# Performance work log

Measured on AMD Instinct MI355X. Metric: run time of the kernel, lower is better.

Reference implementation:

```python
import jax, jax.numpy as jnp
import numpy as np

HID, NH, HD, MD = 512, 8, 64, 16  # hidden_dim, num_heads, head_dim, manifold_dim
B, S = 4, 1024
FLOW_STEPS, DT = 10, 0.1
EPS = 1e-8


def _cplx_weight(k, shape, std=0.02):
    kr, ki = jax.random.split(k)
    w = jax.random.normal(kr, shape) + 1j * jax.random.normal(ki, shape)
    return (w * std).astype(jnp.complex64)


def setup_inputs() -> dict:
    key = jax.random.key(0)
    ks = jax.random.split(key, 12)
    inp = {}
    inp['x_real'] = jax.random.normal(ks[0], (B, S, HID), dtype=jnp.float32)
    inp['x_imag'] = jax.random.normal(ks[1], (B, S, HID), dtype=jnp.float32)
    # manifold projection head_dim -> manifold_dim
    inp['Wm'] = _cplx_weight(ks[2], (MD, HD), std=HD ** -0.5)
    inp['bm'] = jnp.zeros((MD,), jnp.complex64)
    inp['Wq'] = _cplx_weight(ks[3], (MD, MD))
    inp['bq'] = jnp.zeros((MD,), jnp.complex64)
    inp['Wk'] = _cplx_weight(ks[4], (MD, MD))
    inp['bk'] = jnp.zeros((MD,), jnp.complex64)
    inp['Wv'] = _cplx_weight(ks[5], (MD, MD))
    inp['bv'] = jnp.zeros((MD,), jnp.complex64)
    # learned manifold metric (initialized to identity as in the module)
    inp['metric'] = jnp.eye(MD, dtype=jnp.complex64)
    # output projection expanded_dim = NH*MD -> hidden_dim
    inp['Wo'] = _cplx_weight(ks[6], (HID, NH * MD))
    inp['bo'] = jnp.zeros((HID,), jnp.complex64)
    return inp


def _forward(x_real, x_imag, Wm, bm, Wq, bq, Wk, bk, Wv, bv, metric, Wo, bo):
    x = (x_real + 1j * x_imag).astype(jnp.complex64)            # [B,S,HID]
    b, s, _ = x.shape
    h = x.reshape(b, s, NH, HD).transpose(0, 2, 1, 3)           # [B,NH,S,HD]
    # project onto low-dim manifold coordinates
    m = h @ Wm.T + bm                                           # [B,NH,S,MD]
    # hyperbolic exponential map at origin (curvature -1): tanh(|v|)/|v| * v
    n = jnp.sqrt(jnp.sum(jnp.abs(m) ** 2, -1, keepdims=True)) + EPS
    m = (jnp.tanh(n) / n) * m
    # parallel transport via the learned metric
    m = m @ metric
    # geometric flow: 10 Euler integration steps with dt=0.1
    sym = 0.5 * (metric + metric.conj().T)

    def step(carry, _):
        vel = carry @ sym - carry
        return carry + DT * vel, None

    m, _ = jax.lax.scan(step, m, None, length=FLOW_STEPS)
    # hyperbolic logarithm map at origin: artanh(|u|)/|u| * u
    n2 = jnp.sqrt(jnp.sum(jnp.abs(m) ** 2, -1, keepdims=True))
    n2 = jnp.clip(n2, EPS, 1.0 - 1e-6)
    m = (jnp.arctanh(n2) / n2) * m
    # complex q/k/v attention on manifold coordinates
    q = m @ Wq.T + bq
    k = m @ Wk.T + bk
    v = m @ Wv.T + bv
    scale = HD ** -0.5  # module uses self.scale = head_dim ** -0.5
    scores = jnp.einsum('bhsd,bhtd->bhst', q, jnp.conj(k)).real * scale  # [B,NH,S,S]
    attn = jax.nn.softmax(scores, axis=-1).astype(jnp.complex64)
    out = jnp.einsum('bhst,bhtd->bhsd', attn, v)                # [B,NH,S,MD]
    expanded = out.transpose(0, 2, 1, 3).reshape(b, s, NH * MD)  # [B,S,NH*MD]
    return expanded @ Wo.T + bo + x                              # residual, [B,S,HID]


def reference(x_real, x_imag, Wm, bm, Wq, bq, Wk, bk, Wv, bv, metric, Wo, bo):
    return _forward(x_real, x_imag, Wm, bm, Wq, bq, Wk, bk, Wv, bv, metric, Wo, bo)
```

## Files before the change

kernel.cpp:

```cpp
#include <hip/hip_runtime.h>
#include <math.h>

#define HIDD 512
#define NHH 8
#define HDD 64
#define MDD 16
#define Bz 4
#define Sz 1024
#define DTf 0.1f
#define EPSf 1e-8f
#define SCALEf 0.125f

typedef unsigned short ushort_t;
typedef unsigned int uint_t;

typedef __attribute__((ext_vector_type(8))) short bf16x8;
typedef __attribute__((ext_vector_type(4))) float f32x4;

constexpr size_t OFF_QB   = 0;
constexpr size_t OFF_KB   = OFF_QB + 262144;
constexpr size_t OFF_VT   = OFF_KB + 262144;
constexpr size_t OFF_E    = OFF_VT + 262144;
constexpr size_t OFF_WOT  = OFF_E + (size_t)Bz * Sz * NHH * MDD;

__device__ __forceinline__ float bf2f(ushort_t u) {
  union { unsigned int i; float f; } c;
  c.i = ((unsigned int)u) << 16;
  return c.f;
}
__device__ __forceinline__ ushort_t f2bf(float f) {
  unsigned int x = __float_as_uint(f);
  unsigned int r = (x + 0x7fffu + ((x >> 16) & 1u)) >> 16;
  return (ushort_t)r;
}
__device__ __forceinline__ float2 ldc(const void* p, int i, bool bf) {
  if (bf) {
    ushort2 u = ((const ushort2*)p)[i];
    return make_float2(bf2f(u.x), bf2f(u.y));
  }
  return ((const float2*)p)[i];
}
__device__ __forceinline__ float ldr(const void* p, size_t i, bool bf) {
  if (bf) return bf2f(((const ushort_t*)p)[i]);
  return ((const float*)p)[i];
}
__device__ __forceinline__ float2 cmadd(float2 acc, float2 a, float2 b) {
  acc.x = fmaf(a.x, b.x, fmaf(-a.y, b.y, acc.x));
  acc.y = fmaf(a.x, b.y, fmaf(a.y, b.x, acc.y));
  return acc;
}

__global__ __launch_bounds__(256) void k_qkv(
    const void* __restrict__ xr, const void* __restrict__ xi,
    const void* __restrict__ Wm, const void* __restrict__ bm,
    const void* __restrict__ Wq, const void* __restrict__ bq,
    const void* __restrict__ Wk, const void* __restrict__ bk,
    const void* __restrict__ Wv, const void* __restrict__ bv,
    const void* __restrict__ metric,
    ushort_t* __restrict__ Qb, ushort_t* __restrict__ Kb,
    ushort_t* __restrict__ VTb) {
  __shared__ float2 hs[64 * 65];
  __shared__ float2 msc[64 * 17];
  __shared__ float2 wmt[64 * 16];
  __shared__ float2 Tm[256];
  __shared__ float2 wqt[256], wkt[256], wvt[256];
  __shared__ float2 bms[16], bqs[16], bks[16], bvs[16];
  __shared__ int votes[4];
  float2* msc2 = hs;

  int tid = threadIdx.x;
  int bh = blockIdx.y;
  int s0 = blockIdx.x * 64;

  const uint_t* mu = (const uint_t*)metric;
  bool cbf = (mu[0] == 0x00003F80u);

  {
    unsigned e = (((const ushort_t*)xr)[tid] >> 7) & 0xFFu;
    unsigned long long bal = __ballot(e >= 100u && e <= 134u);
    if ((tid & 63) == 0) votes[tid >> 6] = (int)__popcll(bal);
  }

  {
    int i = tid >> 4, j = tid & 15;
    wqt[tid] = ldc(metric, tid, cbf);
    __syncthreads();
    float2 a = wqt[tid];
    float2 bt = wqt[j * 16 + i];
    float2 symv = make_float2(0.5f * (a.x + bt.x), 0.5f * (a.y - bt.y));
    float2 Mv = make_float2(DTf * symv.x, DTf * symv.y);
    if (i == j) Mv.x += 1.0f - DTf;
    wkt[tid] = Mv;
    wvt[tid] = Mv;
    __syncthreads();
    for (int it = 0; it < 9; it++) {
      float2 acc = make_float2(0.f, 0.f);
      #pragma unroll
      for (int k = 0; k < 16; k++) acc = cmadd(acc, wvt[i * 16 + k], wkt[k * 16 + j]);
      __syncthreads();
      wvt[tid] = acc;
      __syncthreads();
    }
    float2 acc = make_float2(0.f, 0.f);
    #pragma unroll
    for (int k = 0; k < 16; k++) acc = cmadd(acc, wqt[i * 16 + k], wvt[k * 16 + j]);
    Tm[tid] = acc;
    __syncthreads();
  }
  bool xbf = (votes[0] + votes[1] + votes[2] + votes[3]) > 192;

  size_t xoff = ((size_t)(((bh >> 3) * Sz) + s0)) * HIDD + (bh & 7) * HDD;
  if (xbf) {
    const ushort_t* xrb = (const ushort_t*)xr + xoff;
    const ushort_t* xib = (const ushort_t*)xi + xoff;
    #pragma unroll
    for (int it = 0; it < 4; it++) {
      int idx = tid + it * 256;
      int i = idx >> 4, e4 = idx & 15;
      ushort4 ur = ((const ushort4*)(xrb + (size_t)i * HIDD))[e4];
      ushort4 ui = ((const ushort4*)(xib + (size_t)i * HIDD))[e4];
      int e = e4 * 4;
      hs[i * 65 + e + 0] = make_float2(bf2f(ur.x), bf2f(ui.x));
      hs[i * 65 + e + 1] = make_float2(bf2f(ur.y), bf2f(ui.y));
      hs[i * 65 + e + 2] = make_float2(bf2f(ur.z), bf2f(ui.z));
      hs[i * 65 + e + 3] = make_float2(bf2f(ur.w), bf2f(ui.w));
    }
  } else {
    const float* xrb = (const float*)xr + xoff;
    const float* xib = (const float*)xi + xoff;
    #pragma unroll
    for (int it = 0; it < 4; it++) {
      int idx = tid + it * 256;
      int i = idx >> 4, e4 = idx & 15;
      float4 fr = ((const float4*)(xrb + (size_t)i * HIDD))[e4];
      float4 fi = ((const float4*)(xib + (size_t)i * HIDD))[e4];
      int e = e4 * 4;
      hs[i * 65 + e + 0] = make_float2(fr.x, fi.x);
      hs[i * 65 + e + 1] = make_float2(fr.y, fi.y);
      hs[i * 65 + e + 2] = make_float2(fr.z, fi.z);
      hs[i * 65 + e + 3] = make_float2(fr.w, fi.w);
    }
  }
  #pragma unroll
  for (int it = 0; it < 4; it++) {
    int c = tid + it * 256;
    int d = c >> 6, e = c & 63;
    wmt[e * 16 + d] = ldc(Wm, c, cbf);
  }
  {
    int j = tid >> 4, d = tid & 15;
    wqt[d * 16 + j] = ldc(Wq, tid, cbf);
    wkt[d * 16 + j] = ldc(Wk, tid, cbf);
    wvt[d * 16 + j] = ldc(Wv, tid, cbf);
    if (tid < 16) {
      bms[tid] = ldc(bm, tid, cbf); bqs[tid] = ldc(bq, tid, cbf);
      bks[tid] = ldc(bk, tid, cbf); bvs[tid] = ldc(bv, tid, cbf);
    }
  }
  __syncthreads();

  int tok = tid >> 2, g = tid & 3;
  int jb = g * 4;

  float2 acc[4];
  #pragma unroll
  for (int i2 = 0; i2 < 4; i2++) acc[i2] = bms[jb + i2];
  for (int e = 0; e < 64; e++) {
    float2 hv = hs[tok * 65 + e];
    #pragma unroll
    for (int i2 = 0; i2 < 4; i2++) acc[i2] = cmadd(acc[i2], hv, wmt[e * 16 + jb + i2]);
  }
  float nn = 0.f;
  #pragma unroll
  for (int i2 = 0; i2 < 4; i2++) nn += acc[i2].x * acc[i2].x + acc[i2].y * acc[i2].y;
  nn += __shfl_xor(nn, 1);
  nn += __shfl_xor(nn, 2);
  float n1 = sqrtf(nn) + EPSf;
  float te = __expf(2.f * n1);
  float sc1 = (te - 1.f) / ((te + 1.f) * n1);
  #pragma unroll
  for (int i2 = 0; i2 < 4; i2++)
    msc[tok * 17 + jb + i2] = make_float2(acc[i2].x * sc1, acc[i2].y * sc1);
  __syncthreads();

  float2 m2[4];
  #pragma unroll
  for (int i2 = 0; i2 < 4; i2++) m2[i2] = make_float2(0.f, 0.f);
  for (int d = 0; d < 16; d++) {
    float2 mv = msc[tok * 17 + d];
    #pragma unroll
    for (int i2 = 0; i2 < 4; i2++) m2[i2] = cmadd(m2[i2], mv, Tm[d * 16 + jb + i2]);
  }
  float nn2 = 0.f;
  #pragma unroll
  for (int i2 = 0; i2 < 4; i2++) nn2 += m2[i2].x * m2[i2].x + m2[i2].y * m2[i2].y;
  nn2 += __shfl_xor(nn2, 1);
  nn2 += __shfl_xor(nn2, 2);
  float n2 = sqrtf(nn2);
  n2 = fminf(fmaxf(n2, EPSf), 1.0f - 1e-6f);
  float fac = 0.5f * __logf((1.f + n2) / (1.f - n2)) / n2;
  #pragma unroll
  for (int i2 = 0; i2 < 4; i2++)
    msc2[tok * 17 + jb + i2] = make_float2(m2[i2].x * fac, m2[i2].y * fac);
  __syncthreads();

  float2 qa[4], ka[4], va[4];
  #pragma unroll
  for (int i2 = 0; i2 < 4; i2++) { qa[i2] = bqs[jb + i2]; ka[i2] = bks[jb + i2]; va[i2] = bvs[jb + i2]; }
  for (int d = 0; d < 16; d++) {
    float2 mv = msc2[tok * 17 + d];
    #pragma unroll
    for (int i2 = 0; i2 < 4; i2++) {
      qa[i2] = cmadd(qa[i2], mv, wqt[d * 16 + jb + i2]);
      ka[i2] = cmadd(ka[i2], mv, wkt[d * 16 + jb + i2]);
      va[i2] = cmadd(va[i2], mv, wvt[d * 16 + jb + i2]);
    }
  }
  int s = s0 + tok;
  uint_t qp[4], kp[4];
  #pragma unroll
  for (int i2 = 0; i2 < 4; i2++) {
    qp[i2] = (uint_t)f2bf(qa[i2].x * SCALEf) | ((uint_t)f2bf(qa[i2].y * SCALEf) << 16);
    kp[i2] = (uint_t)f2bf(ka[i2].x) | ((uint_t)f2bf(ka[i2].y) << 16);
  }
  size_t rowbase = ((size_t)bh * Sz + s) * 32 + (size_t)g * 8;
  *(uint4*)(Qb + rowbase) = make_uint4(qp[0], qp[1], qp[2], qp[3]);
  *(uint4*)(Kb + rowbase) = make_uint4(kp[0], kp[1], kp[2], kp[3]);
  size_t vtb = (size_t)bh * 32 * Sz;
  #pragma unroll
  for (int i2 = 0; i2 < 4; i2++) {
    int d = (jb + i2) * 2;
    VTb[vtb + (size_t)d * Sz + s]       = f2bf(va[i2].x);
    VTb[vtb + (size_t)(d + 1) * Sz + s] = f2bf(va[i2].y);
  }
}

__global__ __launch_bounds__(256) void k_attn_mf(const ushort_t* __restrict__ Qb,
                                                 const ushort_t* __restrict__ Kb,
                                                 const ushort_t* __restrict__ VTb,
                                                 float* __restrict__ ef,
                                                 const void* __restrict__ Wo,
                                                 float2* __restrict__ WoT,
                                                 const void* __restrict__ metric) {
  __shared__ ushort_t Ks[128 * 88];
  __shared__ ushort_t VTs[32 * 152];
  __shared__ ushort_t Ps[4 * 16 * 136];
  int tid = threadIdx.x;

  {
    bool cbf = (((const uint_t*)metric)[0] == 0x00003F80u);
    if (tid < 128) {
      int idx = (blockIdx.y * 16 + blockIdx.x) * 128 + tid;
      int o = idx >> 7, j = idx & 127;
      WoT[(size_t)j * 512 + o] = ldc(Wo, idx, cbf);
    }
  }

  int w = tid >> 6, lane = tid & 63;
  int n = lane & 15, qd = lane >> 4;
  int bh = blockIdx.y;
  int qb = blockIdx.x * 64 + w * 16;

  const ushort_t* Qh = Qb + (size_t)bh * Sz * 32;
  const ushort_t* Kh = Kb + (size_t)bh * Sz * 32;
  const ushort_t* VTh = VTb + (size_t)bh * 32 * Sz;

  bf16x8 qf = *(const bf16x8*)(Qh + (size_t)(qb + n) * 32 + qd * 8);

  f32x4 o0 = {0.f, 0.f, 0.f, 0.f}, o1 = {0.f, 0.f, 0.f, 0.f};
  float m_run = 0.f, l_run = 0.f;
  ushort_t* Pw = Ps + w * 16 * 136;

  for (int kc = 0; kc < Sz; kc += 128) {
    __syncthreads();
    {
      int row = tid >> 1, half = tid & 1;
      const uint4* sk = (const uint4*)(Kh + (size_t)(kc + row) * 32 + half * 16);
      uint4 a = sk[0], b2 = sk[1];
      *(uint4*)(Ks + row * 88 + half * 16) = a;
      *(uint4*)(Ks + row * 88 + half * 16 + 8) = b2;
      int d = tid >> 3, seg = tid & 7;
      const uint4* sv = (const uint4*)(VTh + (size_t)d * Sz + kc + seg * 16);
      uint4 c = sv[0], e2 = sv[1];
      *(uint4*)(VTs + d * 152 + seg * 16) = c;
      *(uint4*)(VTs + d * 152 + seg * 16 + 8) = e2;
    }
    __syncthreads();

    f32x4 st[8];
    __builtin_amdgcn_s_setprio(1);
    #pragma unroll
    for (int s = 0; s < 4; s++) {
      bf16x8 ka0 = *(const bf16x8*)(Ks + (s * 32 + n) * 88 + qd * 8);
      bf16x8 ka1 = *(const bf16x8*)(Ks + (s * 32 + 16 + n) * 88 + qd * 8);
      f32x4 z = {0.f, 0.f, 0.f, 0.f};
      st[2 * s]     = __builtin_amdgcn_mfma_f32_16x16x32_bf16(ka0, qf, z, 0, 0, 0);
      st[2 * s + 1] = __builtin_amdgcn_mfma_f32_16x16x32_bf16(ka1, qf, z, 0, 0, 0);
    }
    __builtin_amdgcn_s_setprio(0);

    float mt = st[0][0];
    #pragma unroll
    for (int i = 0; i < 8; i++) {
      #pragma unroll
      for (int r = 0; r < 4; r++) mt = fmaxf(mt, st[i][r]);
    }
    mt = fmaxf(mt, __shfl_xor(mt, 16));
    mt = fmaxf(mt, __shfl_xor(mt, 32));
    if (!__all(mt - m_run <= 8.f)) {
      float mnew = fmaxf(m_run, mt);
      float alpha = __expf(m_run - mnew);
      l_run *= alpha;
      float ar0 = __shfl(alpha, qd * 4 + 0);
      float ar1 = __shfl(alpha, qd * 4 + 1);
      float ar2 = __shfl(alpha, qd * 4 + 2);
      float ar3 = __shfl(alpha, qd * 4 + 3);
      o0[0] *= ar0; o0[1] *= ar1; o0[2] *= ar2; o0[3] *= ar3;
      o1[0] *= ar0; o1[1] *= ar1; o1[2] *= ar2; o1[3] *= ar3;
      m_run = mnew;
    }

    float lt = 0.f;
    #pragma unroll
    for (int s = 0; s < 4; s++) {
      float p0[4], p1[4];
      #pragma unroll
      for (int r = 0; r < 4; r++) {
        p0[r] = __expf(st[2 * s][r] - m_run);
        p1[r] = __expf(st[2 * s + 1][r] - m_run);
        lt += p0[r] + p1[r];
      }
      uint2 w0, w1;
      w0.x = (uint_t)f2bf(p0[0]) | ((uint_t)f2bf(p0[1]) << 16);
      w0.y = (uint_t)f2bf(p0[2]) | ((uint_t)f2bf(p0[3]) << 16);
      w1.x = (uint_t)f2bf(p1[0]) | ((uint_t)f2bf(p1[1]) << 16);
      w1.y = (uint_t)f2bf(p1[2]) | ((uint_t)f2bf(p1[3]) << 16);
      *(uint2*)(Pw + n * 136 + s * 32 + qd * 4) = w0;
      *(uint2*)(Pw + n * 136 + s * 32 + 16 + qd * 4) = w1;
    }
    l_run += lt;

    __builtin_amdgcn_s_setprio(1);
    #pragma unroll
    for (int s = 0; s < 4; s++) {
      bf16x8 pa  = *(const bf16x8*)(Pw + n * 136 + s * 32 + qd * 8);
      bf16x8 vb0 = *(const bf16x8*)(VTs + n * 152 + s * 32 + qd * 8);
      bf16x8 vb1 = *(const bf16x8*)(VTs + (n + 16) * 152 + s * 32 + qd * 8);
      o0 = __builtin_amdgcn_mfma_f32_16x16x32_bf16(pa, vb0, o0, 0, 0, 0);
      o1 = __builtin_amdgcn_mfma_f32_16x16x32_bf16(pa, vb1, o1, 0, 0, 0);
    }
    __builtin_amdgcn_s_setprio(0);
  }

  l_run += __shfl_xor(l_run, 16);
  l_run += __shfl_xor(l_run, 32);
  int b = bh >> 3, h = bh & 7;
  #pragma unroll
  for (int r = 0; r < 4; r++) {
    float li = __shfl(l_run, qd * 4 + r);
    float inv = 1.0f / li;
    int tok = qb + qd * 4 + r;
    float* ep = ef + (((size_t)(b * Sz + tok)) * NHH + h) * 32;
    ep[n]      = o0[r] * inv;
    ep[16 + n] = o1[r] * inv;
  }
}

__global__ __launch_bounds__(256) void k_proj_r(const float2* __restrict__ ew,
                                                const float2* __restrict__ WoT,
                                                const void* __restrict__ bo,
                                                const void* __restrict__ xr,
                                                const void* __restrict__ metric,
                                                float* __restrict__ out) {
  __shared__ float2 es[8 * 128];
  __shared__ int votes[4];
  int tid = threadIdx.x;
  bool cbf = (((const uint_t*)metric)[0] == 0x00003F80u);
  {
    unsigned e = (((const ushort_t*)xr)[tid] >> 7) & 0xFFu;
    unsigned long long bal = __ballot(e >= 100u && e <= 134u);
    if ((tid & 63) == 0) votes[tid >> 6] = (int)__popcll(bal);
  }
  int tok0 = (blockIdx.x >> 1) * 8;
  int o = (blockIdx.x & 1) * 256 + tid;
  #pragma unroll
  for (int it = 0; it < 4; it++) {
    int idx = tid + it * 256;
    es[idx] = ew[(size_t)tok0 * 128 + idx];
  }
  __syncthreads();
  bool xbf = (votes[0] + votes[1] + votes[2] + votes[3]) > 192;
  float acc[8];
  #pragma unroll
  for (int t = 0; t < 8; t++) acc[t] = 0.f;
  #pragma unroll 8
  for (int j = 0; j < 128; j++) {
    float2 w = WoT[(size_t)j * 512 + o];
    #pragma unroll
    for (int t = 0; t < 8; t++) {
      float2 e = es[t * 128 + j];
      acc[t] = fmaf(e.x, w.x, fmaf(-e.y, w.y, acc[t]));
    }
  }
  float bor = ldc(bo, o, cbf).x;
  #pragma unroll
  for (int t = 0; t < 8; t++) {
    size_t gt = tok0 + t;
    out[gt * HIDD + o] = acc[t] + bor + ldr(xr, gt * HIDD + o, xbf);
  }
}

__global__ __launch_bounds__(256) void k_proj_c(const float2* __restrict__ ew,
                                                const float2* __restrict__ WoT,
                                                const void* __restrict__ bo,
                                                const void* __restrict__ xr,
                                                const void* __restrict__ xi,
                                                const void* __restrict__ metric,
                                                ushort2* __restrict__ out) {
  __shared__ float2 es[8 * 128];
  __shared__ int votes[4];
  int tid = threadIdx.x;
  bool cbf = (((const uint_t*)metric)[0] == 0x00003F80u);
  {
    unsigned e = (((const ushort_t*)xr)[tid] >> 7) & 0xFFu;
    unsigned long long bal = __ballot(e >= 100u && e <= 134u);
    if ((tid & 63) == 0) votes[tid >> 6] = (int)__popcll(bal);
  }
  int tok0 = blockIdx.x * 8;
  #pragma unroll
  for (int it = 0; it < 4; it++) {
    int idx = tid + it * 256;
    es[idx] = ew[(size_t)tok0 * 128 + idx];
  }
  __syncthreads();
  bool xbf = (votes[0] + votes[1] + votes[2] + votes[3]) > 192;
  for (int rep = 0; rep < 2; rep++) {
    int o = tid + rep * 256;
    float2 accT[8];
    #pragma unroll
    for (int t = 0; t < 8; t++) accT[t] = make_float2(0.f, 0.f);
    #pragma unroll 2
    for (int j = 0; j < 128; j++) {
      float2 wv = WoT[(size_t)j * 512 + o];
      #pragma unroll
      for (int t = 0; t < 8; t++) accT[t] = cmadd(accT[t], es[t * 128 + j], wv);
    }
    float2 bov = ldc(bo, o, cbf);
    #pragma unroll
    for (int t = 0; t < 8; t++) {
      size_t gt = tok0 + t;
      float rx = accT[t].x + bov.x + ldr(xr, gt * HIDD + o, xbf);
      float ry = accT[t].y + bov.y + ldr(xi, gt * HIDD + o, xbf);
      out[gt * HIDD + o] = make_ushort2(f2bf(ry), f2bf(rx));
    }
  }
}

extern "C" void kernel_launch(void* const* d_in, const int* in_sizes, int n_in,
                              void* d_out, int out_size, void* d_ws, size_t ws_size,
                              hipStream_t stream) {
  const void* xr     = d_in[0];
  const void* xi     = d_in[1];
  const void* Wm     = d_in[2];
  const void* bm     = d_in[3];
  const void* Wq     = d_in[4];
  const void* bq     = d_in[5];
  const void* Wk     = d_in[6];
  const void* bk     = d_in[7];
  const void* Wv     = d_in[8];
  const void* bv     = d_in[9];
  const void* metric = d_in[10];
  const void* Wo     = d_in[11];
  const void* bo     = d_in[12];

  float2* W = (float2*)d_ws;
  ushort_t* Qb  = (ushort_t*)(W + OFF_QB);
  ushort_t* Kb  = (ushort_t*)(W + OFF_KB);
  ushort_t* VTb = (ushort_t*)(W + OFF_VT);

  k_qkv<<<dim3(16, 32), 256, 0, stream>>>(xr, xi, Wm, bm, Wq, bq, Wk, bk, Wv, bv,
                                          metric, Qb, Kb, VTb);
  k_attn_mf<<<dim3(16, 32), 256, 0, stream>>>(Qb, Kb, VTb, (float*)(W + OFF_E),
                                              Wo, W + OFF_WOT, metric);
  if (out_size == Bz * Sz * HIDD) {
    k_proj_r<<<1024, 256, 0, stream>>>(W + OFF_E, W + OFF_WOT, bo, xr, metric,
                                       (float*)d_out);
  } else {
    k_proj_c<<<512, 256, 0, stream>>>(W + OFF_E, W + OFF_WOT, bo, xr, xi, metric,
                                      (ushort2*)d_out);
  }
}
```

Measured before the change: 149.3 us.

## Use bf16 MFMA for output projection and square metric flow matrix power

For the real-output path, the attention kernel now writes bf16 attention outputs in a token-major layout and a bf16 conjugated Wo, and a new MFMA kernel replaces the scalar FP32 output projection. In the QKV kernel, the matrix ninth power is computed by repeated squaring instead of nine sequential multiplies, and the x loads are issued into registers before the metric work so their latency overlaps it. The goal is to cut the FP32 ALU cost of the projection and the synchronisation-heavy prologue, at the cost of bf16 rounding in the projection inputs.

```diff
diff --git a/kernel.cpp b/kernel.cpp
--- a/kernel.cpp
+++ b/kernel.cpp
@@ -74,6 +74,7 @@
 
   const uint_t* mu = (const uint_t*)metric;
   bool cbf = (mu[0] == 0x00003F80u);
+  int ti = tid >> 4, tj = tid & 15;
 
   {
     unsigned e = (((const ushort_t*)xr)[tid] >> 7) & 0xFFu;
@@ -81,80 +82,104 @@
     if ((tid & 63) == 0) votes[tid >> 6] = (int)__popcll(bal);
   }
 
-  {
-    int i = tid >> 4, j = tid & 15;
-    wqt[tid] = ldc(metric, tid, cbf);
-    __syncthreads();
-    float2 a = wqt[tid];
-    float2 bt = wqt[j * 16 + i];
-    float2 symv = make_float2(0.5f * (a.x + bt.x), 0.5f * (a.y - bt.y));
-    float2 Mv = make_float2(DTf * symv.x, DTf * symv.y);
-    if (i == j) Mv.x += 1.0f - DTf;
-    wkt[tid] = Mv;
-    wvt[tid] = Mv;
-    __syncthreads();
-    for (int it = 0; it < 9; it++) {
-      float2 acc = make_float2(0.f, 0.f);
-      #pragma unroll
-      for (int k = 0; k < 16; k++) acc = cmadd(acc, wvt[i * 16 + k], wkt[k * 16 + j]);
-      __syncthreads();
-      wvt[tid] = acc;
-      __syncthreads();
-    }
-    float2 acc = make_float2(0.f, 0.f);
-    #pragma unroll
-    for (int k = 0; k < 16; k++) acc = cmadd(acc, wqt[i * 16 + k], wvt[k * 16 + j]);
-    Tm[tid] = acc;
-    __syncthreads();
-  }
-  bool xbf = (votes[0] + votes[1] + votes[2] + votes[3]) > 192;
-
-  size_t xoff = ((size_t)(((bh >> 3) * Sz) + s0)) * HIDD + (bh & 7) * HDD;
-  if (xbf) {
-    const ushort_t* xrb = (const ushort_t*)xr + xoff;
-    const ushort_t* xib = (const ushort_t*)xi + xoff;
-    #pragma unroll
-    for (int it = 0; it < 4; it++) {
-      int idx = tid + it * 256;
-      int i = idx >> 4, e4 = idx & 15;
-      ushort4 ur = ((const ushort4*)(xrb + (size_t)i * HIDD))[e4];
-      ushort4 ui = ((const ushort4*)(xib + (size_t)i * HIDD))[e4];
-      int e = e4 * 4;
-      hs[i * 65 + e + 0] = make_float2(bf2f(ur.x), bf2f(ui.x));
-      hs[i * 65 + e + 1] = make_float2(bf2f(ur.y), bf2f(ui.y));
-      hs[i * 65 + e + 2] = make_float2(bf2f(ur.z), bf2f(ui.z));
-      hs[i * 65 + e + 3] = make_float2(bf2f(ur.w), bf2f(ui.w));
-    }
-  } else {
-    const float* xrb = (const float*)xr + xoff;
-    const float* xib = (const float*)xi + xoff;
-    #pragma unroll
-    for (int it = 0; it < 4; it++) {
-      int idx = tid + it * 256;
-      int i = idx >> 4, e4 = idx & 15;
-      float4 fr = ((const float4*)(xrb + (size_t)i * HIDD))[e4];
-      float4 fi = ((const float4*)(xib + (size_t)i * HIDD))[e4];
-      int e = e4 * 4;
-      hs[i * 65 + e + 0] = make_float2(fr.x, fi.x);
-      hs[i * 65 + e + 1] = make_float2(fr.y, fi.y);
-      hs[i * 65 + e + 2] = make_float2(fr.z, fi.z);
-      hs[i * 65 + e + 3] = make_float2(fr.w, fi.w);
-    }
-  }
+  wqt[tid] = ldc(metric, tid, cbf);
   #pragma unroll
   for (int it = 0; it < 4; it++) {
     int c = tid + it * 256;
     int d = c >> 6, e = c & 63;
     wmt[e * 16 + d] = ldc(Wm, c, cbf);
   }
+  float2 wq_r = ldc(Wq, tid, cbf);
+  float2 wk_r = ldc(Wk, tid, cbf);
+  float2 wv_r = ldc(Wv, tid, cbf);
+  float2 bm_r = make_float2(0.f, 0.f), bq_r = bm_r, bk_r = bm_r, bv_r = bm_r;
+  if (tid < 16) {
+    bm_r = ldc(bm, tid, cbf); bq_r = ldc(bq, tid, cbf);
+    bk_r = ldc(bk, tid, cbf); bv_r = ldc(bv, tid, cbf);
+  }
+  __syncthreads();
+  bool xbf = (votes[0] + votes[1] + votes[2] + votes[3]) > 192;
+
+  size_t xoff = ((size_t)(((bh >> 3) * Sz) + s0)) * HIDD + (bh & 7) * HDD;
+  ushort4 xur[4], xui[4];
+  float4 xfr[4], xfi[4];
+  if (xbf) {
+    const ushort_t* xrb = (const ushort_t*)xr + xoff;
+    const ushort_t* xib = (const ushort_t*)xi + xoff;
+    #pragma unroll
+    for (int it = 0; it < 4; it++) {
+      int idx = tid + it * 256;
+      int i = idx >> 4, e4 = idx & 15;
+      xur[it] = ((const ushort4*)(xrb + (size_t)i * HIDD))[e4];
+      xui[it] = ((const ushort4*)(xib + (size_t)i * HIDD))[e4];
+    }
+  } else {
+    const float* xrb = (const float*)xr + xoff;
+    const float* xib = (const float*)xi + xoff;
+    #pragma unroll
+    for (int it = 0; it < 4; it++) {
+      int idx = tid + it * 256;
+      int i = idx >> 4, e4 = idx & 15;
+      xfr[it] = ((const float4*)(xrb + (size_t)i * HIDD))[e4];
+      xfi[it] = ((const float4*)(xib + (size_t)i * HIDD))[e4];
+    }
+  }
+
+  #define MATMUL16(DST, S1, S2)                                              \
+    {                                                                        \
+      float2 acc_ = make_float2(0.f, 0.f);                                   \
+      _Pragma("unroll")                                                      \
+      for (int k_ = 0; k_ < 16; k_++)                                        \
+        acc_ = cmadd(acc_, S1[ti * 16 + k_], S2[k_ * 16 + tj]);              \
+      DST[tid] = acc_;                                                       \
+    }
   {
-    int j = tid >> 4, d = tid & 15;
-    wqt[d * 16 + j] = ldc(Wq, tid, cbf);
-    wkt[d * 16 + j] = ldc(Wk, tid, cbf);
-    wvt[d * 16 + j] = ldc(Wv, tid, cbf);
-    if (tid < 16) {
-      bms[tid] = ldc(bm, tid, cbf); bqs[tid] = ldc(bq, tid, cbf);
-      bks[tid] = ldc(bk, tid, cbf); bvs[tid] = ldc(bv, tid, cbf);
+    float2 a = wqt[tid];
+    float2 bt = wqt[tj * 16 + ti];
+    float2 symv = make_float2(0.5f * (a.x + bt.x), 0.5f * (a.y - bt.y));
+    float2 Mv = make_float2(DTf * symv.x, DTf * symv.y);
+    if (ti == tj) Mv.x += 1.0f - DTf;
+    wkt[tid] = Mv;
+  }
+  __syncthreads();
+  MATMUL16(wvt, wkt, wkt);
+  __syncthreads();
+  MATMUL16(Tm, wvt, wvt);
+  __syncthreads();
+  MATMUL16(wvt, Tm, wkt);
+  __syncthreads();
+  MATMUL16(Tm, wvt, wvt);
+  __syncthreads();
+  float2 Tacc = make_float2(0.f, 0.f);
+  #pragma unroll
+  for (int k = 0; k < 16; k++) Tacc = cmadd(Tacc, wqt[ti * 16 + k], Tm[k * 16 + tj]);
+  __syncthreads();
+  #undef MATMUL16
+
+  Tm[tid] = Tacc;
+  wqt[tj * 16 + ti] = wq_r;
+  wkt[tj * 16 + ti] = wk_r;
+  wvt[tj * 16 + ti] = wv_r;
+  if (tid < 16) { bms[tid] = bm_r; bqs[tid] = bq_r; bks[tid] = bk_r; bvs[tid] = bv_r; }
+  if (xbf) {
+    #pragma unroll
+    for (int it = 0; it < 4; it++) {
+      int idx = tid + it * 256;
+      int i = idx >> 4, e = (idx & 15) * 4;
+      hs[i * 65 + e + 0] = make_float2(bf2f(xur[it].x), bf2f(xui[it].x));
+      hs[i * 65 + e + 1] = make_float2(bf2f(xur[it].y), bf2f(xui[it].y));
+      hs[i * 65 + e + 2] = make_float2(bf2f(xur[it].z), bf2f(xui[it].z));
+      hs[i * 65 + e + 3] = make_float2(bf2f(xur[it].w), bf2f(xui[it].w));
+    }
+  } else {
+    #pragma unroll
+    for (int it = 0; it < 4; it++) {
+      int idx = tid + it * 256;
+      int i = idx >> 4, e = (idx & 15) * 4;
+      hs[i * 65 + e + 0] = make_float2(xfr[it].x, xfi[it].x);
+      hs[i * 65 + e + 1] = make_float2(xfr[it].y, xfi[it].y);
+      hs[i * 65 + e + 2] = make_float2(xfr[it].z, xfi[it].z);
+      hs[i * 65 + e + 3] = make_float2(xfr[it].w, xfi[it].w);
     }
   }
   __syncthreads();
@@ -241,7 +266,10 @@
                                                  float* __restrict__ ef,
                                                  const void* __restrict__ Wo,
                                                  float2* __restrict__ WoT,
-                                                 const void* __restrict__ metric) {
+                                                 ushort_t* __restrict__ Ab,
+                                                 ushort_t* __restrict__ Bb,
+                                                 const void* __restrict__ metric,
+                                                 int cmode) {
   __shared__ ushort_t Ks[128 * 88];
   __shared__ ushort_t VTs[32 * 152];
   __shared__ ushort_t Ps[4 * 16 * 136];
@@ -251,8 +279,13 @@
     bool cbf = (((const uint_t*)metric)[0] == 0x00003F80u);
     if (tid < 128) {
       int idx = (blockIdx.y * 16 + blockIdx.x) * 128 + tid;
-      int o = idx >> 7, j = idx & 127;
-      WoT[(size_t)j * 512 + o] = ldc(Wo, idx, cbf);
+      float2 wv = ldc(Wo, idx, cbf);
+      if (cmode) {
+        int o = idx >> 7, j = idx & 127;
+        WoT[(size_t)j * 512 + o] = wv;
+      } else {
+        ((ushort2*)Bb)[idx] = make_ushort2(f2bf(wv.x), f2bf(-wv.y));
+      }
     }
   }
 
@@ -355,24 +388,34 @@
   l_run += __shfl_xor(l_run, 16);
   l_run += __shfl_xor(l_run, 32);
   int b = bh >> 3, h = bh & 7;
-  #pragma unroll
-  for (int r = 0; r < 4; r++) {
-    float li = __shfl(l_run, qd * 4 + r);
-    float inv = 1.0f / li;
-    int tok = qb + qd * 4 + r;
-    float* ep = ef + (((size_t)(b * Sz + tok)) * NHH + h) * 32;
-    ep[n]      = o0[r] * inv;
-    ep[16 + n] = o1[r] * inv;
-  }
-}
-
-__global__ __launch_bounds__(256) void k_proj_r(const float2* __restrict__ ew,
-                                                const float2* __restrict__ WoT,
-                                                const void* __restrict__ bo,
-                                                const void* __restrict__ xr,
-                                                const void* __restrict__ metric,
-                                                float* __restrict__ out) {
-  __shared__ float2 es[8 * 128];
+  if (cmode == 0) {
+    #pragma unroll
+    for (int r = 0; r < 4; r++) {
+      float li = __shfl(l_run, qd * 4 + r);
+      float inv = 1.0f / li;
+      size_t gt = (size_t)(b * Sz + qb + qd * 4 + r);
+      Ab[gt * 256 + h * 32 + n]      = f2bf(o0[r] * inv);
+      Ab[gt * 256 + h * 32 + 16 + n] = f2bf(o1[r] * inv);
+    }
+  } else {
+    #pragma unroll
+    for (int r = 0; r < 4; r++) {
+      float li = __shfl(l_run, qd * 4 + r);
+      float inv = 1.0f / li;
+      int tok = qb + qd * 4 + r;
+      float* ep = ef + (((size_t)(b * Sz + tok)) * NHH + h) * 32;
+      ep[n]      = o0[r] * inv;
+      ep[16 + n] = o1[r] * inv;
+    }
+  }
+}
+
+__global__ __launch_bounds__(256) void k_proj_mf(const ushort_t* __restrict__ Ab,
+                                                 const ushort_t* __restrict__ Bb,
+                                                 const void* __restrict__ bo,
+                                                 const void* __restrict__ xr,
+                                                 const void* __restrict__ metric,
+                                                 float* __restrict__ out) {
   __shared__ int votes[4];
   int tid = threadIdx.x;
   bool cbf = (((const uint_t*)metric)[0] == 0x00003F80u);
@@ -381,32 +424,35 @@
     unsigned long long bal = __ballot(e >= 100u && e <= 134u);
     if ((tid & 63) == 0) votes[tid >> 6] = (int)__popcll(bal);
   }
-  int tok0 = (blockIdx.x >> 1) * 8;
-  int o = (blockIdx.x & 1) * 256 + tid;
-  #pragma unroll
-  for (int it = 0; it < 4; it++) {
-    int idx = tid + it * 256;
-    es[idx] = ew[(size_t)tok0 * 128 + idx];
-  }
   __syncthreads();
   bool xbf = (votes[0] + votes[1] + votes[2] + votes[3]) > 192;
-  float acc[8];
-  #pragma unroll
-  for (int t = 0; t < 8; t++) acc[t] = 0.f;
-  #pragma unroll 8
-  for (int j = 0; j < 128; j++) {
-    float2 w = WoT[(size_t)j * 512 + o];
-    #pragma unroll
-    for (int t = 0; t < 8; t++) {
-      float2 e = es[t * 128 + j];
-      acc[t] = fmaf(e.x, w.x, fmaf(-e.y, w.y, acc[t]));
-    }
-  }
-  float bor = ldc(bo, o, cbf).x;
-  #pragma unroll
-  for (int t = 0; t < 8; t++) {
-    size_t gt = tok0 + t;
-    out[gt * HIDD + o] = acc[t] + bor + ldr(xr, gt * HIDD + o, xbf);
+
+  int w = tid >> 6, lane = tid & 63;
+  int n = lane & 15, qd = lane >> 4;
+  int tb = blockIdx.x * 16;
+  int ob = blockIdx.y * 256 + w * 64;
+
+  bf16x8 af[8];
+  const ushort_t* Ar = Ab + (size_t)(tb + n) * 256 + qd * 8;
+  #pragma unroll
+  for (int ks = 0; ks < 8; ks++) af[ks] = *(const bf16x8*)(Ar + ks * 32);
+
+  #pragma unroll
+  for (int nt = 0; nt < 4; nt++) {
+    int o = ob + nt * 16 + n;
+    const ushort_t* Br = Bb + (size_t)o * 256 + qd * 8;
+    f32x4 c = {0.f, 0.f, 0.f, 0.f};
+    #pragma unroll
+    for (int ks = 0; ks < 8; ks++) {
+      bf16x8 bfr = *(const bf16x8*)(Br + ks * 32);
+      c = __builtin_amdgcn_mfma_f32_16x16x32_bf16(bfr, af[ks], c, 0, 0, 0);
+    }
+    float bor = ldc(bo, o, cbf).x;
+    #pragma unroll
+    for (int r = 0; r < 4; r++) {
+      size_t gt = (size_t)(tb + qd * 4 + r);
+      out[gt * HIDD + o] = c[r] + bor + ldr(xr, gt * HIDD + o, xbf);
+    }
   }
 }
 
@@ -477,14 +523,18 @@
   ushort_t* Qb  = (ushort_t*)(W + OFF_QB);
   ushort_t* Kb  = (ushort_t*)(W + OFF_KB);
   ushort_t* VTb = (ushort_t*)(W + OFF_VT);
+  ushort_t* Ab  = (ushort_t*)(W + OFF_E);
+  ushort_t* Bb  = (ushort_t*)(W + OFF_WOT);
+
+  int cmode = (out_size == Bz * Sz * HIDD) ? 0 : 1;
 
   k_qkv<<<dim3(16, 32), 256, 0, stream>>>(xr, xi, Wm, bm, Wq, bq, Wk, bk, Wv, bv,
                                           metric, Qb, Kb, VTb);
   k_attn_mf<<<dim3(16, 32), 256, 0, stream>>>(Qb, Kb, VTb, (float*)(W + OFF_E),
-                                              Wo, W + OFF_WOT, metric);
-  if (out_size == Bz * Sz * HIDD) {
-    k_proj_r<<<1024, 256, 0, stream>>>(W + OFF_E, W + OFF_WOT, bo, xr, metric,
-                                       (float*)d_out);
+                                              Wo, W + OFF_WOT, Ab, Bb, metric, cmode);
+  if (cmode == 0) {
+    k_proj_mf<<<dim3(256, 2), 256, 0, stream>>>(Ab, Bb, bo, xr, metric,
+                                                (float*)d_out);
   } else {
     k_proj_c<<<512, 256, 0, stream>>>(W + OFF_E, W + OFF_WOT, bo, xr, xi, metric,
                                       (ushort2*)d_out);
```

New measurement: 136.1 us. 1.1x faster.
